# Kernel tuning notes

Hardware: AMD Instinct MI355X
Metric: run time of the kernel (lower is better)

## Reference

```python
import jax, jax.numpy as jnp
import numpy as np

TQ, TK, H, HEADS = 2048, 2048, 1024, 16

def setup_inputs() -> dict:
    key = jax.random.key(0)
    ks = jax.random.split(key, 11)
    s = 1.0 / np.sqrt(H).astype(np.float32)
    return {
        "Q": jax.random.normal(ks[0], (TQ, H), jnp.float32),
        "K": jax.random.normal(ks[1], (TK, H), jnp.float32),
        "V": jax.random.normal(ks[2], (TK, H), jnp.float32),
        "Wq": jax.random.normal(ks[3], (H, H), jnp.float32) * s,
        "bq": jax.random.normal(ks[4], (H,), jnp.float32) * s,
        "Wk": jax.random.normal(ks[5], (H, H), jnp.float32) * s,
        "bk": jax.random.normal(ks[6], (H,), jnp.float32) * s,
        "Wv": jax.random.normal(ks[7], (H, H), jnp.float32) * s,
        "bv": jax.random.normal(ks[8], (H,), jnp.float32) * s,
        # linear_out: nn.Linear(num_heads, 1) -> weight [num_heads], bias scalar
        "Wo": jax.random.normal(ks[9], (HEADS,), jnp.float32) / np.sqrt(HEADS).astype(np.float32),
        "bo": jax.random.normal(ks[10], (), jnp.float32) / np.sqrt(HEADS).astype(np.float32),
    }

def reference(Q, K, V, Wq, bq, Wk, bk, Wv, bv, Wo, bo):
    heads = Wo.shape[0]
    # relu(linear) projections
    Q_l = jax.nn.relu(Q @ Wq.T + bq)            # [Tq, H]
    K_l = jax.nn.relu(K @ Wk.T + bk)            # [Tk, H]
    V_l = jax.nn.relu(V @ Wv.T + bv)            # [Tk, H]
    Tq, Hd = Q_l.shape
    Tk = K_l.shape[0]
    d = Hd // heads                              # head dim
    Qh = Q_l.reshape(Tq, heads, d)               # split heads (torch split+cat over dim0)
    Kh = K_l.reshape(Tk, heads, d)
    # per-head scaled scores: [Tq, Tk, heads]
    scale = np.float32(1.0 / np.sqrt(d))
    scores = jnp.einsum('qhd,khd->qkh', Qh, Kh) * scale
    # learned linear combine over heads -> [Tq, Tk]
    logits = scores @ Wo + bo
    attn = jax.nn.softmax(logits, axis=1)        # softmax over Tk
    out = attn @ V_l                             # [Tq, H]
    return out, attn.T                           # attention.transpose(1,0) -> [Tk, Tq]
```

## Files before the change

### kernel.cpp

```cpp
#include <hip/hip_runtime.h>
#include <stdint.h>


#define TQ 2048
#define TK 2048
#define HD 1024

#define DEVI __device__ __forceinline__

typedef __attribute__((ext_vector_type(8))) short bf16x8;
typedef __attribute__((ext_vector_type(4))) float f32x4;
typedef __attribute__((ext_vector_type(4))) unsigned short u16x4;
typedef unsigned short ushort_t;

DEVI unsigned short f2bf(float f) {
  uint32_t u = __builtin_bit_cast(uint32_t, f);
  u += 0x7FFFu + ((u >> 16) & 1u);
  return (unsigned short)(u >> 16);
}
DEVI float bf2f(unsigned short h) {
  uint32_t u = ((uint32_t)h) << 16;
  return __builtin_bit_cast(float, u);
}

DEVI void gload_lds16(const void* g, void* l) {
  __builtin_amdgcn_global_load_lds((const __attribute__((address_space(1))) void*)g,
                                   (__attribute__((address_space(3))) void*)l,
                                   16, 0, 0);
}

DEVI void stage_tiles(const unsigned short* __restrict__ Ab, const unsigned short* __restrict__ Bb,
                      int lda, int ldb, int k0,
                      unsigned short* lA, unsigned short* lB, int tid) {
#pragma unroll
  for (int i = 0; i < 2; i++) {
    int c = i * 512 + tid;
    int r = c >> 3;
    int cs = (c & 7) ^ (r & 7);
    gload_lds16(Ab + (size_t)r * lda + k0 + cs * 8, lA + c * 8);
    gload_lds16(Bb + (size_t)r * ldb + k0 + cs * 8, lB + c * 8);
  }
}

DEVI void compute_kt(const unsigned short* lA, const unsigned short* lB,
                     f32x4 acc[4][2], int wr, int wc, int l15, int hi) {
#pragma unroll
  for (int kk = 0; kk < 2; kk++) {
    bf16x8 af[4], bfr[2];
#pragma unroll
    for (int f = 0; f < 4; f++) {
      int ra = wr * 64 + f * 16 + l15;
      int ca = (kk * 4 + hi) ^ (ra & 7);
      af[f] = *(const bf16x8*)(lA + ra * 64 + ca * 8);
    }
#pragma unroll
    for (int f = 0; f < 2; f++) {
      int rb = wc * 32 + f * 16 + l15;
      int cb = (kk * 4 + hi) ^ (rb & 7);
      bfr[f] = *(const bf16x8*)(lB + rb * 64 + cb * 8);
    }
#pragma unroll
    for (int fm = 0; fm < 4; fm++)
#pragma unroll
      for (int fn = 0; fn < 2; fn++)
        acc[fm][fn] = __builtin_amdgcn_mfma_f32_16x16x32_bf16(af[fm], bfr[fn], acc[fm][fn], 0, 0, 0);
  }
}

DEVI void mfma_loop_db(const unsigned short* __restrict__ A, const unsigned short* __restrict__ B,
                       int lda, int ldb, int K, unsigned short* lds, f32x4 acc[4][2]) {
  const int tid = threadIdx.x;
  const int lane = tid & 63;
  const int wave = tid >> 6;
  const int wr = wave >> 2, wc = wave & 3;
  const int l15 = lane & 15, hi = lane >> 4;

#pragma unroll
  for (int i = 0; i < 4; i++)
#pragma unroll
    for (int j = 0; j < 2; j++) acc[i][j] = (f32x4)(0.0f);

  unsigned short* lA0 = lds;
  unsigned short* lB0 = lds + 8192;
  unsigned short* lA1 = lds + 16384;
  unsigned short* lB1 = lds + 24576;

  const int nkt = K >> 6;
  stage_tiles(A, B, lda, ldb, 0, lA0, lB0, tid);
  __syncthreads();
  for (int kt = 0; kt < nkt; kt += 2) {
    if (kt + 1 < nkt) stage_tiles(A, B, lda, ldb, (kt + 1) * 64, lA1, lB1, tid);
    compute_kt(lA0, lB0, acc, wr, wc, l15, hi);
    __syncthreads();
    if (kt + 1 < nkt) {
      if (kt + 2 < nkt) stage_tiles(A, B, lda, ldb, (kt + 2) * 64, lA0, lB0, tid);
      compute_kt(lA1, lB1, acc, wr, wc, l15, hi);
      __syncthreads();
    }
  }
}

DEVI void xcd_decode_16x16(int d, int& bm, int& bn) {
  int x = d & 7, j = d >> 3;
  bm = ((x >> 1) << 2) + (j >> 3);
  bn = ((x & 1) << 3) + (j & 7);
}
DEVI void xcd_decode_16x8(int d, int& bm, int& bn) {
  int x = d & 7, j = d >> 3;
  bm = ((x >> 1) << 2) + (j >> 2);
  bn = ((x & 1) << 2) + (j & 3);
}

__global__ __launch_bounds__(512)
void gemm_logits(const unsigned short* __restrict__ Ql, const unsigned short* __restrict__ Ks,
                 float* __restrict__ C) {
  __shared__ __align__(16) unsigned short lds[32768];
  int bm, bn;
  xcd_decode_16x16(blockIdx.x, bm, bn);
  f32x4 acc[4][2];
  mfma_loop_db(Ql + (size_t)bm * 128 * HD, Ks + (size_t)bn * 128 * HD, HD, HD, HD, lds, acc);

  const int tid = threadIdx.x;
  const int lane = tid & 63, wave = tid >> 6;
  const int wr = wave >> 2, wc = wave & 3;
  const int l15 = lane & 15, hi = lane >> 4;
  const int row0 = bm * 128 + wr * 64;
  const int col0 = bn * 128 + wc * 32;
#pragma unroll
  for (int fm = 0; fm < 4; fm++)
#pragma unroll
    for (int fn = 0; fn < 2; fn++) {
      int cg = col0 + fn * 16 + l15;
      int rg = row0 + fm * 16 + hi * 4;
#pragma unroll
      for (int i = 0; i < 4; i++)
        C[(size_t)(rg + i) * TK + cg] = acc[fm][fn][i];
    }
}

__global__ __launch_bounds__(512)
void gemm_pv(const unsigned short* __restrict__ attnb, const unsigned short* __restrict__ VT,
             float* __restrict__ part) {
  __shared__ __align__(16) unsigned short lds[32768];
  int bm, bn;
  xcd_decode_16x8(blockIdx.x, bm, bn);
  const int ks = blockIdx.y;
  f32x4 acc[4][2];
  mfma_loop_db(attnb + (size_t)bm * 128 * TK + ks * 1024,
               VT + (size_t)bn * 128 * TK + ks * 1024, TK, TK, 1024, lds, acc);

  float* Cp = part + (size_t)ks * TQ * HD;
  const int tid = threadIdx.x;
  const int lane = tid & 63, wave = tid >> 6;
  const int wr = wave >> 2, wc = wave & 3;
  const int l15 = lane & 15, hi = lane >> 4;
  const int row0 = bm * 128 + wr * 64;
  const int col0 = bn * 128 + wc * 32;
#pragma unroll
  for (int fm = 0; fm < 4; fm++)
#pragma unroll
    for (int fn = 0; fn < 2; fn++) {
      int cg = col0 + fn * 16 + l15;
      int rg = row0 + fm * 16 + hi * 4;
#pragma unroll
      for (int i = 0; i < 4; i++)
        Cp[(size_t)(rg + i) * HD + cg] = acc[fm][fn][i];
    }
}

__global__ __launch_bounds__(512)
void gemm_proj(const unsigned short* __restrict__ Qb, const unsigned short* __restrict__ Kb,
               const unsigned short* __restrict__ Vb,
               const unsigned short* __restrict__ Wqb, const unsigned short* __restrict__ Wkb,
               const unsigned short* __restrict__ Wvb,
               const float* __restrict__ bq, const float* __restrict__ bk,
               const float* __restrict__ bv, const float* __restrict__ Wo,
               unsigned short* __restrict__ Ql, unsigned short* __restrict__ Ks,
               unsigned short* __restrict__ VT) {
  __shared__ __align__(16) unsigned short lds[32768];
  const int z = blockIdx.y;
  const unsigned short* A = (z == 0) ? Qb : (z == 1) ? Kb : Vb;
  const unsigned short* B = (z == 0) ? Wqb : (z == 1) ? Wkb : Wvb;
  const float* bias = (z == 0) ? bq : (z == 1) ? bk : bv;

  int bm, bn;
  xcd_decode_16x8(blockIdx.x, bm, bn);
  f32x4 acc[4][2];
  mfma_loop_db(A + (size_t)bm * 128 * HD, B + (size_t)bn * 128 * HD, HD, HD, HD, lds, acc);

  const int tid = threadIdx.x;
  const int lane = tid & 63, wave = tid >> 6;
  const int wr = wave >> 2, wc = wave & 3;
  const int l15 = lane & 15, hi = lane >> 4;
  const int row0 = bm * 128 + wr * 64;
  const int col0 = bn * 128 + wc * 32;

#pragma unroll
  for (int fm = 0; fm < 4; fm++)
#pragma unroll
    for (int fn = 0; fn < 2; fn++) {
      int cg = col0 + fn * 16 + l15;
      int rg = row0 + fm * 16 + hi * 4;
      float b = bias[cg];
      if (z == 2) {
        u16x4 o;
#pragma unroll
        for (int i = 0; i < 4; i++) o[i] = f2bf(fmaxf(acc[fm][fn][i] + b, 0.0f));
        *(u16x4*)(VT + (size_t)cg * TK + rg) = o;
      } else if (z == 1) {
        float s = 0.125f * Wo[cg >> 6];
#pragma unroll
        for (int i = 0; i < 4; i++)
          Ks[(size_t)(rg + i) * HD + cg] = f2bf(fmaxf(acc[fm][fn][i] + b, 0.0f) * s);
      } else {
#pragma unroll
        for (int i = 0; i < 4; i++)
          Ql[(size_t)(rg + i) * HD + cg] = f2bf(fmaxf(acc[fm][fn][i] + b, 0.0f));
      }
    }
}

__global__ __launch_bounds__(256)
void softmax_k(const float* __restrict__ logits, unsigned short* __restrict__ attnb) {
  const int row = blockIdx.x;
  const int tid = threadIdx.x;
  const int lane = tid & 63;
  const int wave = tid >> 6;
  const float* lr = logits + (size_t)row * TK;

  f32x4 v0 = *(const f32x4*)(lr + tid * 8);
  f32x4 v1 = *(const f32x4*)(lr + tid * 8 + 4);
  float x[8];
#pragma unroll
  for (int j = 0; j < 4; j++) { x[j] = v0[j]; x[4 + j] = v1[j]; }

  float m = x[0];
#pragma unroll
  for (int j = 1; j < 8; j++) m = fmaxf(m, x[j]);
  for (int o = 32; o > 0; o >>= 1) m = fmaxf(m, __shfl_xor(m, o));
  __shared__ float redm[4], reds[4];
  if (lane == 0) redm[wave] = m;
  __syncthreads();
  m = fmaxf(fmaxf(redm[0], redm[1]), fmaxf(redm[2], redm[3]));

  const float L2E = 1.44269504088896341f;
  float e[8];
  float s = 0.0f;
#pragma unroll
  for (int j = 0; j < 8; j++) { e[j] = exp2f((x[j] - m) * L2E); s += e[j]; }
  for (int o = 32; o > 0; o >>= 1) s += __shfl_xor(s, o);
  if (lane == 0) reds[wave] = s;
  __syncthreads();
  s = reds[0] + reds[1] + reds[2] + reds[3];
  float inv = 1.0f / s;

  unsigned short* ar = attnb + (size_t)row * TK;
  u16x4 o0, o1;
#pragma unroll
  for (int j = 0; j < 4; j++) { o0[j] = f2bf(e[j] * inv); o1[j] = f2bf(e[4 + j] * inv); }
  *(u16x4*)(ar + tid * 8) = o0;
  *(u16x4*)(ar + tid * 8 + 4) = o1;
}

__global__ __launch_bounds__(256)
void transpose_attn(const unsigned short* __restrict__ attnb, float* __restrict__ attnT) {
  __shared__ unsigned short tile[64][68];
  const int tr = blockIdx.y * 64;
  const int tc = blockIdx.x * 64;
  const int tid = threadIdx.x;
#pragma unroll
  for (int i = 0; i < 4; i++) {
    int q = i * 256 + tid;
    int r = q >> 4;
    int c4 = (q & 15) * 4;
    u16x4 v = *(const u16x4*)(attnb + (size_t)(tr + r) * TK + tc + c4);
    *(u16x4*)(&tile[r][c4]) = v;
  }
  __syncthreads();
#pragma unroll
  for (int i = 0; i < 4; i++) {
    int q = i * 256 + tid;
    int c = q >> 4;
    int r4 = (q & 15) * 4;
    f32x4 o;
#pragma unroll
    for (int j = 0; j < 4; j++) o[j] = bf2f(tile[r4 + j][c]);
    *(f32x4*)(attnT + (size_t)(tc + c) * TQ + tr + r4) = o;
  }
}

__global__ __launch_bounds__(256)
void cvt3(const float* __restrict__ a, const float* __restrict__ b, const float* __restrict__ c,
          unsigned short* __restrict__ da, unsigned short* __restrict__ db,
          unsigned short* __restrict__ dc, int n4) {
  const int z = blockIdx.y;
  const float* s = (z == 0) ? a : (z == 1) ? b : c;
  unsigned short* d = (z == 0) ? da : (z == 1) ? db : dc;
  int i = blockIdx.x * 256 + threadIdx.x;
  if (i < n4) {
    f32x4 v = *(const f32x4*)(s + i * 4);
    u16x4 o;
#pragma unroll
    for (int j = 0; j < 4; j++) o[j] = f2bf(v[j]);
    *(u16x4*)(d + i * 4) = o;
  }
}

__global__ __launch_bounds__(256)
void reduce_add(const float* __restrict__ p0, const float* __restrict__ p1,
                float* __restrict__ out, int n4) {
  int i = blockIdx.x * 256 + threadIdx.x;
  if (i < n4) {
    f32x4 a = *(const f32x4*)(p0 + i * 4);
    f32x4 b = *(const f32x4*)(p1 + i * 4);
    f32x4 o;
#pragma unroll
    for (int j = 0; j < 4; j++) o[j] = a[j] + b[j];
    *(f32x4*)(out + i * 4) = o;
  }
}

extern "C" void kernel_launch(void* const* d_in, const int* in_sizes, int n_in,
                              void* d_out, int out_size, void* d_ws, size_t ws_size,
                              hipStream_t stream) {
  const float* Q  = (const float*)d_in[0];
  const float* K  = (const float*)d_in[1];
  const float* V  = (const float*)d_in[2];
  const float* Wq = (const float*)d_in[3];
  const float* bq = (const float*)d_in[4];
  const float* Wk = (const float*)d_in[5];
  const float* bk = (const float*)d_in[6];
  const float* Wv = (const float*)d_in[7];
  const float* bv = (const float*)d_in[8];
  const float* Wo = (const float*)d_in[9];

  uint8_t* w = (uint8_t*)d_ws;
  unsigned short* Qb  = (unsigned short*)(w + 0);
  unsigned short* Kb  = (unsigned short*)(w + 4194304);
  unsigned short* Vb  = (unsigned short*)(w + 8388608);
  unsigned short* Wqb = (unsigned short*)(w + 12582912);
  unsigned short* Wkb = (unsigned short*)(w + 14680064);
  unsigned short* Wvb = (unsigned short*)(w + 16777216);
  unsigned short* Ql  = (unsigned short*)(w + 18874368);
  unsigned short* Ks  = (unsigned short*)(w + 23068672);
  unsigned short* VT  = (unsigned short*)(w + 27262976);
  float*          logits = (float*)(w + 31457280);
  unsigned short* attnb  = (unsigned short*)(w + 48234496);
  float* p0 = (float*)(w + 0);
  float* p1 = (float*)(w + 8388608);

  float* outp  = (float*)d_out;
  float* attnT = outp + (size_t)TQ * HD;

  cvt3<<<dim3(2048, 3), dim3(256), 0, stream>>>(Q, K, V, Qb, Kb, Vb, TQ * HD / 4);
  cvt3<<<dim3(1024, 3), dim3(256), 0, stream>>>(Wq, Wk, Wv, Wqb, Wkb, Wvb, HD * HD / 4);

  gemm_proj<<<dim3(128, 3), dim3(512), 0, stream>>>(Qb, Kb, Vb, Wqb, Wkb, Wvb,
                                                    bq, bk, bv, Wo, Ql, Ks, VT);

  gemm_logits<<<dim3(256), dim3(512), 0, stream>>>(Ql, Ks, logits);

  softmax_k<<<dim3(TQ), dim3(256), 0, stream>>>(logits, attnb);

  gemm_pv<<<dim3(128, 2), dim3(512), 0, stream>>>(attnb, VT, p0);
  reduce_add<<<dim3(2048), dim3(256), 0, stream>>>(p0, p1, outp, TQ * HD / 4);

  transpose_attn<<<dim3(32, 32), dim3(256), 0, stream>>>(attnb, attnT);
}
```

Before: 83.72 us.

## Use 4-stage async GEMM pipeline, retile projections, fuse PV with transpose

Replaces the double-buffered GEMM loop with a 4-stage LDS pipeline that uses explicit vmcnt waits, raw barriers and raised wave priority during MFMA. The projection GEMM moves to 128x64 tiles over a flat 768-block grid, and the two conversion kernels merge into one. The split-K PV GEMM and its reduce kernel give way to a single full-K PV that shares one launch with the attention transpose. This cuts launches and the partial-sum traffic, and hides global load latency better, at the cost of more LDS per block (lower occupancy) and an uneven mixed grid.

```diff
diff --git a/kernel.cpp b/kernel.cpp
--- a/kernel.cpp
+++ b/kernel.cpp
@@ -22,34 +22,45 @@
   uint32_t u = ((uint32_t)h) << 16;
   return __builtin_bit_cast(float, u);
 }
-
 DEVI void gload_lds16(const void* g, void* l) {
   __builtin_amdgcn_global_load_lds((const __attribute__((address_space(1))) void*)g,
                                    (__attribute__((address_space(3))) void*)l,
                                    16, 0, 0);
 }
-
-DEVI void stage_tiles(const unsigned short* __restrict__ Ab, const unsigned short* __restrict__ Bb,
-                      int lda, int ldb, int k0,
-                      unsigned short* lA, unsigned short* lB, int tid) {
+template<int N> DEVI void wait_vm() { asm volatile("s_waitcnt vmcnt(%0)" :: "n"(N) : "memory"); }
+DEVI void wait_lgkm0() { asm volatile("s_waitcnt lgkmcnt(0)" ::: "memory"); }
+#define SBAR() __builtin_amdgcn_s_barrier()
+
+template<int BN>
+DEVI void stageT(const unsigned short* __restrict__ A, const unsigned short* __restrict__ B,
+                 int lda, int ldb, int k0, unsigned short* buf, int tid) {
 #pragma unroll
   for (int i = 0; i < 2; i++) {
     int c = i * 512 + tid;
     int r = c >> 3;
     int cs = (c & 7) ^ (r & 7);
-    gload_lds16(Ab + (size_t)r * lda + k0 + cs * 8, lA + c * 8);
-    gload_lds16(Bb + (size_t)r * ldb + k0 + cs * 8, lB + c * 8);
-  }
-}
-
-DEVI void compute_kt(const unsigned short* lA, const unsigned short* lB,
-                     f32x4 acc[4][2], int wr, int wc, int l15, int hi) {
+    gload_lds16(A + (size_t)r * lda + k0 + cs * 8, buf + c * 8);
+  }
+#pragma unroll
+  for (int i = 0; i < BN / 64; i++) {
+    int c = i * 512 + tid;
+    int r = c >> 3;
+    int cs = (c & 7) ^ (r & 7);
+    gload_lds16(B + (size_t)r * ldb + k0 + cs * 8, buf + 8192 + c * 8);
+  }
+}
+
+template<int BN>
+DEVI void computeT(const unsigned short* lA, const unsigned short* lB, f32x4 acc[4][2],
+                   int wr, int wc, int l15, int hi) {
+  constexpr int FM = (BN == 128) ? 4 : 2;
+  constexpr int WMR = (BN == 128) ? 64 : 32;
 #pragma unroll
   for (int kk = 0; kk < 2; kk++) {
     bf16x8 af[4], bfr[2];
 #pragma unroll
-    for (int f = 0; f < 4; f++) {
-      int ra = wr * 64 + f * 16 + l15;
+    for (int f = 0; f < FM; f++) {
+      int ra = wr * WMR + f * 16 + l15;
       int ca = (kk * 4 + hi) ^ (ra & 7);
       af[f] = *(const bf16x8*)(lA + ra * 64 + ca * 8);
     }
@@ -60,112 +71,48 @@
       bfr[f] = *(const bf16x8*)(lB + rb * 64 + cb * 8);
     }
 #pragma unroll
-    for (int fm = 0; fm < 4; fm++)
+    for (int fm = 0; fm < FM; fm++)
 #pragma unroll
       for (int fn = 0; fn < 2; fn++)
         acc[fm][fn] = __builtin_amdgcn_mfma_f32_16x16x32_bf16(af[fm], bfr[fn], acc[fm][fn], 0, 0, 0);
   }
 }
 
-DEVI void mfma_loop_db(const unsigned short* __restrict__ A, const unsigned short* __restrict__ B,
-                       int lda, int ldb, int K, unsigned short* lds, f32x4 acc[4][2]) {
-  const int tid = threadIdx.x;
-  const int lane = tid & 63;
-  const int wave = tid >> 6;
-  const int wr = wave >> 2, wc = wave & 3;
+template<int BN, int NKT>
+DEVI void mfma_pipeline(const unsigned short* __restrict__ A, const unsigned short* __restrict__ B,
+                        int lda, int ldb, unsigned short* lds, f32x4 acc[4][2]) {
+  constexpr int FM = (BN == 128) ? 4 : 2;
+  constexpr int LPS = 2 + BN / 64;
+  constexpr int BSTR = 8192 + BN * 64;
+  const int tid = threadIdx.x;
+  const int lane = tid & 63, wave = tid >> 6;
   const int l15 = lane & 15, hi = lane >> 4;
-
-#pragma unroll
-  for (int i = 0; i < 4; i++)
+  const int wr = (BN == 128) ? (wave >> 2) : (wave >> 1);
+  const int wc = (BN == 128) ? (wave & 3) : (wave & 1);
+
+#pragma unroll
+  for (int i = 0; i < FM; i++)
 #pragma unroll
     for (int j = 0; j < 2; j++) acc[i][j] = (f32x4)(0.0f);
 
-  unsigned short* lA0 = lds;
-  unsigned short* lB0 = lds + 8192;
-  unsigned short* lA1 = lds + 16384;
-  unsigned short* lB1 = lds + 24576;
-
-  const int nkt = K >> 6;
-  stage_tiles(A, B, lda, ldb, 0, lA0, lB0, tid);
-  __syncthreads();
-  for (int kt = 0; kt < nkt; kt += 2) {
-    if (kt + 1 < nkt) stage_tiles(A, B, lda, ldb, (kt + 1) * 64, lA1, lB1, tid);
-    compute_kt(lA0, lB0, acc, wr, wc, l15, hi);
-    __syncthreads();
-    if (kt + 1 < nkt) {
-      if (kt + 2 < nkt) stage_tiles(A, B, lda, ldb, (kt + 2) * 64, lA0, lB0, tid);
-      compute_kt(lA1, lB1, acc, wr, wc, l15, hi);
-      __syncthreads();
-    }
-  }
-}
-
-DEVI void xcd_decode_16x16(int d, int& bm, int& bn) {
-  int x = d & 7, j = d >> 3;
-  bm = ((x >> 1) << 2) + (j >> 3);
-  bn = ((x & 1) << 3) + (j & 7);
-}
-DEVI void xcd_decode_16x8(int d, int& bm, int& bn) {
-  int x = d & 7, j = d >> 3;
-  bm = ((x >> 1) << 2) + (j >> 2);
-  bn = ((x & 1) << 2) + (j & 3);
-}
-
-__global__ __launch_bounds__(512)
-void gemm_logits(const unsigned short* __restrict__ Ql, const unsigned short* __restrict__ Ks,
-                 float* __restrict__ C) {
-  __shared__ __align__(16) unsigned short lds[32768];
-  int bm, bn;
-  xcd_decode_16x16(blockIdx.x, bm, bn);
-  f32x4 acc[4][2];
-  mfma_loop_db(Ql + (size_t)bm * 128 * HD, Ks + (size_t)bn * 128 * HD, HD, HD, HD, lds, acc);
-
-  const int tid = threadIdx.x;
-  const int lane = tid & 63, wave = tid >> 6;
-  const int wr = wave >> 2, wc = wave & 3;
-  const int l15 = lane & 15, hi = lane >> 4;
-  const int row0 = bm * 128 + wr * 64;
-  const int col0 = bn * 128 + wc * 32;
-#pragma unroll
-  for (int fm = 0; fm < 4; fm++)
-#pragma unroll
-    for (int fn = 0; fn < 2; fn++) {
-      int cg = col0 + fn * 16 + l15;
-      int rg = row0 + fm * 16 + hi * 4;
-#pragma unroll
-      for (int i = 0; i < 4; i++)
-        C[(size_t)(rg + i) * TK + cg] = acc[fm][fn][i];
-    }
-}
-
-__global__ __launch_bounds__(512)
-void gemm_pv(const unsigned short* __restrict__ attnb, const unsigned short* __restrict__ VT,
-             float* __restrict__ part) {
-  __shared__ __align__(16) unsigned short lds[32768];
-  int bm, bn;
-  xcd_decode_16x8(blockIdx.x, bm, bn);
-  const int ks = blockIdx.y;
-  f32x4 acc[4][2];
-  mfma_loop_db(attnb + (size_t)bm * 128 * TK + ks * 1024,
-               VT + (size_t)bn * 128 * TK + ks * 1024, TK, TK, 1024, lds, acc);
-
-  float* Cp = part + (size_t)ks * TQ * HD;
-  const int tid = threadIdx.x;
-  const int lane = tid & 63, wave = tid >> 6;
-  const int wr = wave >> 2, wc = wave & 3;
-  const int l15 = lane & 15, hi = lane >> 4;
-  const int row0 = bm * 128 + wr * 64;
-  const int col0 = bn * 128 + wc * 32;
-#pragma unroll
-  for (int fm = 0; fm < 4; fm++)
-#pragma unroll
-    for (int fn = 0; fn < 2; fn++) {
-      int cg = col0 + fn * 16 + l15;
-      int rg = row0 + fm * 16 + hi * 4;
-#pragma unroll
-      for (int i = 0; i < 4; i++)
-        Cp[(size_t)(rg + i) * HD + cg] = acc[fm][fn][i];
-    }
+#pragma unroll
+  for (int s = 0; s < 4; s++) stageT<BN>(A, B, lda, ldb, s * 64, lds + s * BSTR, tid);
+
+#pragma unroll 1
+  for (int t = 0; t < NKT; ++t) {
+    if (t < NKT - 3) wait_vm<3 * LPS>();
+    else if (t == NKT - 3) wait_vm<2 * LPS>();
+    else if (t == NKT - 2) wait_vm<LPS>();
+    else wait_vm<0>();
+    SBAR();
+    unsigned short* buf = lds + (t & 3) * BSTR;
+    __builtin_amdgcn_s_setprio(1);
+    computeT<BN>(buf, buf + 8192, acc, wr, wc, l15, hi);
+    __builtin_amdgcn_s_setprio(0);
+    wait_lgkm0();
+    SBAR();
+    if (t + 4 < NKT) stageT<BN>(A, B, lda, ldb, (t + 4) * 64, buf, tid);
+  }
 }
 
 __global__ __launch_bounds__(512)
@@ -177,26 +124,30 @@
                const float* __restrict__ bv, const float* __restrict__ Wo,
                unsigned short* __restrict__ Ql, unsigned short* __restrict__ Ks,
                unsigned short* __restrict__ VT) {
-  __shared__ __align__(16) unsigned short lds[32768];
-  const int z = blockIdx.y;
+  __shared__ __align__(16) unsigned short lds[4 * 12288];
+  const int bid = blockIdx.x;
+  const int x = bid & 7, j = bid >> 3;
+  const int z = j >> 5;
+  const int jj = j & 31;
+  const int bm = (x & 3) * 4 + (jj >> 3);
+  const int bn = (x >> 2) * 8 + (jj & 7);
+
   const unsigned short* A = (z == 0) ? Qb : (z == 1) ? Kb : Vb;
   const unsigned short* B = (z == 0) ? Wqb : (z == 1) ? Wkb : Wvb;
   const float* bias = (z == 0) ? bq : (z == 1) ? bk : bv;
 
-  int bm, bn;
-  xcd_decode_16x8(blockIdx.x, bm, bn);
   f32x4 acc[4][2];
-  mfma_loop_db(A + (size_t)bm * 128 * HD, B + (size_t)bn * 128 * HD, HD, HD, HD, lds, acc);
+  mfma_pipeline<64, 16>(A + (size_t)bm * 128 * HD, B + (size_t)bn * 64 * HD, HD, HD, lds, acc);
 
   const int tid = threadIdx.x;
   const int lane = tid & 63, wave = tid >> 6;
-  const int wr = wave >> 2, wc = wave & 3;
+  const int wr = wave >> 1, wc = wave & 1;
   const int l15 = lane & 15, hi = lane >> 4;
-  const int row0 = bm * 128 + wr * 64;
-  const int col0 = bn * 128 + wc * 32;
-
-#pragma unroll
-  for (int fm = 0; fm < 4; fm++)
+  const int row0 = bm * 128 + wr * 32;
+  const int col0 = bn * 64 + wc * 32;
+
+#pragma unroll
+  for (int fm = 0; fm < 2; fm++)
 #pragma unroll
     for (int fn = 0; fn < 2; fn++) {
       int cg = col0 + fn * 16 + l15;
@@ -220,6 +171,91 @@
     }
 }
 
+__global__ __launch_bounds__(512)
+void gemm_logits(const unsigned short* __restrict__ Ql, const unsigned short* __restrict__ Ks,
+                 float* __restrict__ C) {
+  __shared__ __align__(16) unsigned short lds[4 * 16384];
+  const int bid = blockIdx.x;
+  const int x = bid & 7, j = bid >> 3;
+  const int bm = (x & 3) * 4 + (j >> 3);
+  const int bn = (x >> 2) * 8 + (j & 7);
+
+  f32x4 acc[4][2];
+  mfma_pipeline<128, 16>(Ql + (size_t)bm * 128 * HD, Ks + (size_t)bn * 128 * HD, HD, HD, lds, acc);
+
+  const int tid = threadIdx.x;
+  const int lane = tid & 63, wave = tid >> 6;
+  const int wr = wave >> 2, wc = wave & 3;
+  const int l15 = lane & 15, hi = lane >> 4;
+  const int row0 = bm * 128 + wr * 64;
+  const int col0 = bn * 128 + wc * 32;
+#pragma unroll
+  for (int fm = 0; fm < 4; fm++)
+#pragma unroll
+    for (int fn = 0; fn < 2; fn++) {
+      int cg = col0 + fn * 16 + l15;
+      int rg = row0 + fm * 16 + hi * 4;
+#pragma unroll
+      for (int i = 0; i < 4; i++)
+        C[(size_t)(rg + i) * TK + cg] = acc[fm][fn][i];
+    }
+}
+
+__global__ __launch_bounds__(512)
+void pv_and_transpose(const unsigned short* __restrict__ attnb, const unsigned short* __restrict__ VT,
+                      float* __restrict__ outp, float* __restrict__ attnT) {
+  __shared__ __align__(16) unsigned short lds[4 * 16384];
+  const int bid = blockIdx.x;
+  const int tid = threadIdx.x;
+  if (bid < 128) {
+    const int x = bid & 7, j = bid >> 3;
+    const int bm = (x & 3) * 4 + (j >> 2);
+    const int bn = (x >> 2) * 4 + (j & 3);
+    f32x4 acc[4][2];
+    mfma_pipeline<128, 32>(attnb + (size_t)bm * 128 * TK, VT + (size_t)bn * 128 * TK,
+                           TK, TK, lds, acc);
+    const int lane = tid & 63, wave = tid >> 6;
+    const int wr = wave >> 2, wc = wave & 3;
+    const int l15 = lane & 15, hi = lane >> 4;
+    const int row0 = bm * 128 + wr * 64;
+    const int col0 = bn * 128 + wc * 32;
+#pragma unroll
+    for (int fm = 0; fm < 4; fm++)
+#pragma unroll
+      for (int fn = 0; fn < 2; fn++) {
+        int cg = col0 + fn * 16 + l15;
+        int rg = row0 + fm * 16 + hi * 4;
+#pragma unroll
+        for (int i = 0; i < 4; i++)
+          outp[(size_t)(rg + i) * HD + cg] = acc[fm][fn][i];
+      }
+  } else {
+    unsigned short (*tile)[68] = reinterpret_cast<unsigned short (*)[68]>(lds);
+    const int q0 = bid - 128;
+    const int tr = (q0 >> 5) * 64;
+    const int tc = (q0 & 31) * 64;
+#pragma unroll
+    for (int i = 0; i < 2; i++) {
+      int q = i * 512 + tid;
+      int r = q >> 4;
+      int c4 = (q & 15) * 4;
+      u16x4 v = *(const u16x4*)(attnb + (size_t)(tr + r) * TK + tc + c4);
+      *(u16x4*)(&tile[r][c4]) = v;
+    }
+    __syncthreads();
+#pragma unroll
+    for (int i = 0; i < 2; i++) {
+      int q = i * 512 + tid;
+      int c = q >> 4;
+      int r4 = (q & 15) * 4;
+      f32x4 o;
+#pragma unroll
+      for (int jx = 0; jx < 4; jx++) o[jx] = bf2f(tile[r4 + jx][c]);
+      *(f32x4*)(attnT + (size_t)(tc + c) * TQ + tr + r4) = o;
+    }
+  }
+}
+
 __global__ __launch_bounds__(256)
 void softmax_k(const float* __restrict__ logits, unsigned short* __restrict__ attnb) {
   const int row = blockIdx.x;
@@ -263,39 +299,23 @@
 }
 
 __global__ __launch_bounds__(256)
-void transpose_attn(const unsigned short* __restrict__ attnb, float* __restrict__ attnT) {
-  __shared__ unsigned short tile[64][68];
-  const int tr = blockIdx.y * 64;
-  const int tc = blockIdx.x * 64;
-  const int tid = threadIdx.x;
-#pragma unroll
-  for (int i = 0; i < 4; i++) {
-    int q = i * 256 + tid;
-    int r = q >> 4;
-    int c4 = (q & 15) * 4;
-    u16x4 v = *(const u16x4*)(attnb + (size_t)(tr + r) * TK + tc + c4);
-    *(u16x4*)(&tile[r][c4]) = v;
-  }
-  __syncthreads();
-#pragma unroll
-  for (int i = 0; i < 4; i++) {
-    int q = i * 256 + tid;
-    int c = q >> 4;
-    int r4 = (q & 15) * 4;
-    f32x4 o;
-#pragma unroll
-    for (int j = 0; j < 4; j++) o[j] = bf2f(tile[r4 + j][c]);
-    *(f32x4*)(attnT + (size_t)(tc + c) * TQ + tr + r4) = o;
-  }
-}
-
-__global__ __launch_bounds__(256)
-void cvt3(const float* __restrict__ a, const float* __restrict__ b, const float* __restrict__ c,
-          unsigned short* __restrict__ da, unsigned short* __restrict__ db,
-          unsigned short* __restrict__ dc, int n4) {
-  const int z = blockIdx.y;
-  const float* s = (z == 0) ? a : (z == 1) ? b : c;
-  unsigned short* d = (z == 0) ? da : (z == 1) ? db : dc;
+void cvt6(const float* __restrict__ Q, const float* __restrict__ K, const float* __restrict__ V,
+          const float* __restrict__ Wq, const float* __restrict__ Wk, const float* __restrict__ Wv,
+          unsigned short* __restrict__ Qb, unsigned short* __restrict__ Kb,
+          unsigned short* __restrict__ Vb, unsigned short* __restrict__ Wqb,
+          unsigned short* __restrict__ Wkb, unsigned short* __restrict__ Wvb) {
+  const int y = blockIdx.y;
+  const float* s;
+  unsigned short* d;
+  int n4;
+  switch (y) {
+    case 0: s = Q;  d = Qb;  n4 = TQ * HD / 4; break;
+    case 1: s = K;  d = Kb;  n4 = TK * HD / 4; break;
+    case 2: s = V;  d = Vb;  n4 = TK * HD / 4; break;
+    case 3: s = Wq; d = Wqb; n4 = HD * HD / 4; break;
+    case 4: s = Wk; d = Wkb; n4 = HD * HD / 4; break;
+    default: s = Wv; d = Wvb; n4 = HD * HD / 4; break;
+  }
   int i = blockIdx.x * 256 + threadIdx.x;
   if (i < n4) {
     f32x4 v = *(const f32x4*)(s + i * 4);
@@ -303,20 +323,6 @@
 #pragma unroll
     for (int j = 0; j < 4; j++) o[j] = f2bf(v[j]);
     *(u16x4*)(d + i * 4) = o;
-  }
-}
-
-__global__ __launch_bounds__(256)
-void reduce_add(const float* __restrict__ p0, const float* __restrict__ p1,
-                float* __restrict__ out, int n4) {
-  int i = blockIdx.x * 256 + threadIdx.x;
-  if (i < n4) {
-    f32x4 a = *(const f32x4*)(p0 + i * 4);
-    f32x4 b = *(const f32x4*)(p1 + i * 4);
-    f32x4 o;
-#pragma unroll
-    for (int j = 0; j < 4; j++) o[j] = a[j] + b[j];
-    *(f32x4*)(out + i * 4) = o;
   }
 }
 
@@ -346,24 +352,18 @@
   unsigned short* VT  = (unsigned short*)(w + 27262976);
   float*          logits = (float*)(w + 31457280);
   unsigned short* attnb  = (unsigned short*)(w + 48234496);
-  float* p0 = (float*)(w + 0);
-  float* p1 = (float*)(w + 8388608);
 
   float* outp  = (float*)d_out;
   float* attnT = outp + (size_t)TQ * HD;
 
-  cvt3<<<dim3(2048, 3), dim3(256), 0, stream>>>(Q, K, V, Qb, Kb, Vb, TQ * HD / 4);
-  cvt3<<<dim3(1024, 3), dim3(256), 0, stream>>>(Wq, Wk, Wv, Wqb, Wkb, Wvb, HD * HD / 4);
-
-  gemm_proj<<<dim3(128, 3), dim3(512), 0, stream>>>(Qb, Kb, Vb, Wqb, Wkb, Wvb,
-                                                    bq, bk, bv, Wo, Ql, Ks, VT);
+  cvt6<<<dim3(2048, 6), dim3(256), 0, stream>>>(Q, K, V, Wq, Wk, Wv, Qb, Kb, Vb, Wqb, Wkb, Wvb);
+
+  gemm_proj<<<dim3(768), dim3(512), 0, stream>>>(Qb, Kb, Vb, Wqb, Wkb, Wvb,
+                                                 bq, bk, bv, Wo, Ql, Ks, VT);
 
   gemm_logits<<<dim3(256), dim3(512), 0, stream>>>(Ql, Ks, logits);
 
   softmax_k<<<dim3(TQ), dim3(256), 0, stream>>>(logits, attnb);
 
-  gemm_pv<<<dim3(128, 2), dim3(512), 0, stream>>>(attnb, VT, p0);
-  reduce_add<<<dim3(2048), dim3(256), 0, stream>>>(p0, p1, outp, TQ * HD / 4);
-
-  transpose_attn<<<dim3(32, 32), dim3(256), 0, stream>>>(attnb, attnT);
-}
+  pv_and_transpose<<<dim3(1152), dim3(512), 0, stream>>>(attnb, VT, outp, attnT);
+}
```

Measured after the change: 83.08 us. About the same (-0.8%).
